# Optimization experiments

Hardware: AMD Instinct MI355X
Metric: run time of the kernel (lower is better)

The kernel has to match this reference:

```python
import jax, jax.numpy as jnp
import numpy as np

N, DEG, D = 30000, 32, 128
NEG_SLOPE = 0.01  # F.leaky_relu default


def setup_inputs() -> dict:
    key = jax.random.key(0)
    k1, k2, k3 = jax.random.split(key, 3)
    a1 = jax.random.normal(k1, (N, D), dtype=jnp.float32)
    a2 = jax.random.normal(k2, (N, DEG, D), dtype=jnp.float32)
    ft = jax.random.normal(k3, (N, DEG, D), dtype=jnp.float32)
    return {"a1": a1, "a2": a2, "ft": ft}


def reference(a1, a2, ft):
    # a1: [N, D] broadcast over mailbox dim; a2, ft: [N, DEG, D]
    a = (a1[:, None, :] + a2).sum(axis=-1, keepdims=True)  # [N, DEG, 1]
    e = jax.nn.softmax(jax.nn.leaky_relu(a, NEG_SLOPE), axis=1)  # softmax over neighbors
    # attn_drop == 0.0 -> no dropout (falsy branch in original)
    accum = (e * ft).sum(axis=1)  # [N, D]
    return accum
```

## Files before the change

kernel.cpp:

```cpp
#include <hip/hip_runtime.h>


#define NN 30000
#define DEG 32
#define DD 128
#define NEG_SLOPE 0.01f

__global__ __launch_bounds__(256) void gat_reduce_kernel(
    const float* __restrict__ a1,
    const float* __restrict__ a2,
    const float* __restrict__ ft,
    float* __restrict__ out)
{
    const int n = blockIdx.x;
    const int t = threadIdx.x;
    const int h = t >> 5;
    const int l = t & 31;

    __shared__ float rowsum[33];
    __shared__ float ew[32];
    __shared__ float partial[8][DD];

    const float4* a2v = (const float4*)a2 + (size_t)n * (DEG * DD / 4);
    const float4* ftv = (const float4*)ft + (size_t)n * (DEG * DD / 4);
    const float4* a1v = (const float4*)a1 + (size_t)n * (DD / 4);

    #pragma unroll
    for (int i = 0; i < 4; ++i) {
        const int k = h + 8 * i;
        float4 v = a2v[k * 32 + l];
        float s = v.x + v.y + v.z + v.w;
        #pragma unroll
        for (int m = 16; m >= 1; m >>= 1) s += __shfl_xor(s, m);
        if (l == 0) rowsum[k] = s;
    }
    if (h == 0) {
        float4 v = a1v[l];
        float s = v.x + v.y + v.z + v.w;
        #pragma unroll
        for (int m = 16; m >= 1; m >>= 1) s += __shfl_xor(s, m);
        if (l == 0) rowsum[32] = s;
    }
    __syncthreads();

    if (t < 32) {
        float a = rowsum[t] + rowsum[32];
        float lr = a > 0.0f ? a : NEG_SLOPE * a;
        float m = lr;
        #pragma unroll
        for (int s = 16; s >= 1; s >>= 1) m = fmaxf(m, __shfl_xor(m, s));
        float p = __expf(lr - m);
        float sum = p;
        #pragma unroll
        for (int s = 16; s >= 1; s >>= 1) sum += __shfl_xor(sum, s);
        ew[t] = p / sum;
    }
    __syncthreads();

    float4 acc = make_float4(0.f, 0.f, 0.f, 0.f);
    #pragma unroll
    for (int i = 0; i < 4; ++i) {
        const int k = h + 8 * i;
        const float w = ew[k];
        float4 v = ftv[k * 32 + l];
        acc.x += w * v.x;
        acc.y += w * v.y;
        acc.z += w * v.z;
        acc.w += w * v.w;
    }
    *(float4*)&partial[h][4 * l] = acc;
    __syncthreads();

    if (t < DD) {
        float s = 0.f;
        #pragma unroll
        for (int j = 0; j < 8; ++j) s += partial[j][t];
        out[(size_t)n * DD + t] = s;
    }
}

extern "C" void kernel_launch(void* const* d_in, const int* in_sizes, int n_in,
                              void* d_out, int out_size, void* d_ws, size_t ws_size,
                              hipStream_t stream) {
    const float* a1 = (const float*)d_in[0];
    const float* a2 = (const float*)d_in[1];
    const float* ft = (const float*)d_in[2];
    float* out = (float*)d_out;
    gat_reduce_kernel<<<NN, 256, 0, stream>>>(a1, a2, ft, out);
}
```

Before: 896.2 us.

## Map one node per wavefront and replace shared-memory reductions with shuffles

Each 64-lane wavefront now processes a whole node, with the two 32-lane halves covering alternating neighbor rows. Row sums, the softmax and the final accumulation are all done with register arrays and cross-half shuffles instead of LDS and block barriers. This removes the syncthreads and shared-memory traffic and gives each thread more loads in flight. The cost is higher register use and fewer blocks, each packing four nodes.

```diff
diff --git a/kernel.cpp b/kernel.cpp
--- a/kernel.cpp
+++ b/kernel.cpp
@@ -12,70 +12,66 @@
     const float* __restrict__ ft,
     float* __restrict__ out)
 {
-    const int n = blockIdx.x;
-    const int t = threadIdx.x;
-    const int h = t >> 5;
-    const int l = t & 31;
-
-    __shared__ float rowsum[33];
-    __shared__ float ew[32];
-    __shared__ float partial[8][DD];
+    const int wave = threadIdx.x >> 6;
+    const int lane = threadIdx.x & 63;
+    const int half = lane >> 5;
+    const int l    = lane & 31;
+    const int n    = blockIdx.x * 4 + wave;
 
     const float4* a2v = (const float4*)a2 + (size_t)n * (DEG * DD / 4);
     const float4* ftv = (const float4*)ft + (size_t)n * (DEG * DD / 4);
-    const float4* a1v = (const float4*)a1 + (size_t)n * (DD / 4);
+    const float2* a1v = (const float2*)a1 + (size_t)n * (DD / 2);
 
+    float2 av = a1v[lane];
+    float c = av.x + av.y;
     #pragma unroll
-    for (int i = 0; i < 4; ++i) {
-        const int k = h + 8 * i;
-        float4 v = a2v[k * 32 + l];
+    for (int m = 32; m >= 1; m >>= 1) c += __shfl_xor(c, m);
+
+    float rs[16];
+    #pragma unroll
+    for (int i = 0; i < 16; ++i) {
+        float4 v = a2v[(2 * i + half) * 32 + l];
         float s = v.x + v.y + v.z + v.w;
         #pragma unroll
         for (int m = 16; m >= 1; m >>= 1) s += __shfl_xor(s, m);
-        if (l == 0) rowsum[k] = s;
+        rs[i] = s;
     }
-    if (h == 0) {
-        float4 v = a1v[l];
-        float s = v.x + v.y + v.z + v.w;
-        #pragma unroll
-        for (int m = 16; m >= 1; m >>= 1) s += __shfl_xor(s, m);
-        if (l == 0) rowsum[32] = s;
+
+    float mx = -3.0e38f;
+    #pragma unroll
+    for (int i = 0; i < 16; ++i) {
+        float a  = rs[i] + c;
+        float lr = a > 0.0f ? a : NEG_SLOPE * a;
+        rs[i] = lr;
+        mx = fmaxf(mx, lr);
     }
-    __syncthreads();
-
-    if (t < 32) {
-        float a = rowsum[t] + rowsum[32];
-        float lr = a > 0.0f ? a : NEG_SLOPE * a;
-        float m = lr;
-        #pragma unroll
-        for (int s = 16; s >= 1; s >>= 1) m = fmaxf(m, __shfl_xor(m, s));
-        float p = __expf(lr - m);
-        float sum = p;
-        #pragma unroll
-        for (int s = 16; s >= 1; s >>= 1) sum += __shfl_xor(sum, s);
-        ew[t] = p / sum;
+    mx = fmaxf(mx, __shfl_xor(mx, 32));
+    float ssum = 0.0f;
+    #pragma unroll
+    for (int i = 0; i < 16; ++i) {
+        float p = __expf(rs[i] - mx);
+        rs[i] = p;
+        ssum += p;
     }
-    __syncthreads();
+    ssum += __shfl_xor(ssum, 32);
+    const float inv = 1.0f / ssum;
 
     float4 acc = make_float4(0.f, 0.f, 0.f, 0.f);
     #pragma unroll
-    for (int i = 0; i < 4; ++i) {
-        const int k = h + 8 * i;
-        const float w = ew[k];
-        float4 v = ftv[k * 32 + l];
+    for (int i = 0; i < 16; ++i) {
+        const float w = rs[i] * inv;
+        float4 v = ftv[(2 * i + half) * 32 + l];
         acc.x += w * v.x;
         acc.y += w * v.y;
         acc.z += w * v.z;
         acc.w += w * v.w;
     }
-    *(float4*)&partial[h][4 * l] = acc;
-    __syncthreads();
-
-    if (t < DD) {
-        float s = 0.f;
-        #pragma unroll
-        for (int j = 0; j < 8; ++j) s += partial[j][t];
-        out[(size_t)n * DD + t] = s;
+    acc.x += __shfl_xor(acc.x, 32);
+    acc.y += __shfl_xor(acc.y, 32);
+    acc.z += __shfl_xor(acc.z, 32);
+    acc.w += __shfl_xor(acc.w, 32);
+    if (half == 0) {
+        ((float4*)out)[(size_t)n * 32 + l] = acc;
     }
 }
 
@@ -86,5 +82,5 @@
     const float* a2 = (const float*)d_in[1];
     const float* ft = (const float*)d_in[2];
     float* out = (float*)d_out;
-    gat_reduce_kernel<<<NN, 256, 0, stream>>>(a1, a2, ft, out);
+    gat_reduce_kernel<<<NN / 4, 256, 0, stream>>>(a1, a2, ft, out);
 }
```

After: 902.1 us. Within noise of the previous version (+0.7%).
